# Kernel optimization log

Hardware: AMD Instinct MI355X
Metric: run time of the kernel (lower is better)

## Reference

```python
import jax, jax.numpy as jnp
import numpy as np

# Analytic closed form of the 4-qubit circuit. Wires (0,1) and (2,3) are
# independent 2-qubit blocks: RY(x_a)oRY(x_b) -> CNOT(a,b) -> RY(p_a)oRY(p_b).
# Heisenberg picture gives:
#   <Z_a> = cos(p_a)*cos(x_a) + sin(p_a)*sin(x_a)*sin(x_b)
#   <Z_b> = cos(p_b)*cos(x_a)*cos(x_b) + sin(p_b)*sin(x_b)

def setup_inputs() -> dict:
    key = jax.random.key(0)
    k1, k2, k3, k4 = jax.random.split(key, 4)
    B = 16384
    return {
        "x": jax.random.uniform(k1, (B, 1, 28, 28), dtype=jnp.float32),
        "vqc_params": jax.random.normal(k2, (4,), dtype=jnp.float32),
        "fc_w": jax.random.normal(k3, (10, 784), dtype=jnp.float32) * 0.05,
        "fc_b": jax.random.normal(k4, (10,), dtype=jnp.float32) * 0.05,
        "bias": jnp.zeros((10,), dtype=jnp.float32),
    }


def _pair_expvals(xa, xb, pa, pb):
    # xa, xb: [B, 196]; pa, pb: scalars
    za = jnp.cos(pa) * jnp.cos(xa) + jnp.sin(pa) * jnp.sin(xa) * jnp.sin(xb)
    zb = jnp.cos(pb) * jnp.cos(xa) * jnp.cos(xb) + jnp.sin(pb) * jnp.sin(xb)
    return za, zb


def reference(x, vqc_params, fc_w, fc_b, bias):
    B = x.shape[0]
    # Extract 2x2 patches in the same (r, c) row-major order as the torch loop.
    # [B,28,28] -> [B,14,2,14,2] -> [B,14,14,2,2] -> [B,196,4]
    p = x[:, 0].reshape(B, 14, 2, 14, 2).transpose(0, 1, 3, 2, 4).reshape(B, 196, 4)
    x0, x1, x2, x3 = p[..., 0], p[..., 1], p[..., 2], p[..., 3]
    p0, p1, p2, p3 = vqc_params[0], vqc_params[1], vqc_params[2], vqc_params[3]
    z0, z1 = _pair_expvals(x0, x1, p0, p1)
    z2, z3 = _pair_expvals(x2, x3, p2, p3)
    q = jnp.stack([z0, z1, z2, z3], axis=-1).reshape(B, 4 * 196)  # patch-major, wire-minor
    logits = q @ fc_w.T + fc_b - bias
    return jax.nn.log_softmax(logits, axis=-1)
```

## Files before the change

kernel.cpp:

```cpp
#include <hip/hip_runtime.h>
#include <hip/hip_bf16.h>


typedef __attribute__((ext_vector_type(8))) short short8;
typedef __attribute__((ext_vector_type(4))) float f32x4;

constexpr int WAVES = 4;
constexpr int BLOCK = WAVES * 64;
constexpr int IMGS  = 16;
constexpr int NITER = 7;

static __device__ __forceinline__ short f2bf(float f) {
    union { float f; unsigned u; } v; v.f = f;
    unsigned r = v.u + 0x7fffu + ((v.u >> 16) & 1u);
    return (short)(r >> 16);
}

__global__ __launch_bounds__(BLOCK, 4)
void quanv_mfma(const float* __restrict__ x,
                const float* __restrict__ vqc,
                const float* __restrict__ fc_w,
                const float* __restrict__ fc_b,
                const float* __restrict__ bias,
                float* __restrict__ out,
                int B)
{
    __shared__ float cpart[3][64 * 4];

    const int tid  = threadIdx.x;
    const int lane = tid & 63;
    const int wv   = tid >> 6;
    const int i16  = lane & 15;
    const int g    = lane >> 4;

    const int imgBase = blockIdx.x * IMGS;
    const int imgLane = imgBase + i16;
    const long xb = (long)(imgLane < B ? imgLane : B - 1) * 784;

    float S0, C0, S1, C1, S2, C2, S3, C3;
    __sincosf(vqc[0], &S0, &C0);
    __sincosf(vqc[1], &S1, &C1);
    __sincosf(vqc[2], &S2, &C2);
    __sincosf(vqc[3], &S3, &C3);

    const int ncl = (i16 < 10) ? i16 : 9;
    short8 bf[NITER];
    #pragma unroll
    for (int I = 0; I < NITER; ++I) {
        const int kb = wv + 4 * I;
        int k = kb * 32 + g * 8;
        if (k > 776) k = 776;
        const float4 lo = *reinterpret_cast<const float4*>(fc_w + ncl * 784 + k);
        const float4 hi = *reinterpret_cast<const float4*>(fc_w + ncl * 784 + k + 4);
        short8 t;
        t[0] = f2bf(lo.x); t[1] = f2bf(lo.y); t[2] = f2bf(lo.z); t[3] = f2bf(lo.w);
        t[4] = f2bf(hi.x); t[5] = f2bf(hi.y); t[6] = f2bf(hi.z); t[7] = f2bf(hi.w);
        bf[I] = t;
    }

    auto xoff = [&](int I) -> int {
        const int kb = wv + 4 * I;
        int j0 = kb * 8 + 2 * g;
        if (j0 > 194) j0 = 0;
        const int r = j0 / 14, c = j0 - 14 * r;
        return 56 * r + 2 * c;
    };

    f32x4 acc = {0.f, 0.f, 0.f, 0.f};

    float4 curT = *reinterpret_cast<const float4*>(x + xb + xoff(0));
    float4 curB = *reinterpret_cast<const float4*>(x + xb + xoff(0) + 28);

    #pragma unroll
    for (int I = 0; I < NITER; ++I) {
        float4 nxT, nxB;
        if (I < NITER - 1) {
            const int o = xoff(I + 1);
            nxT = *reinterpret_cast<const float4*>(x + xb + o);
            nxB = *reinterpret_cast<const float4*>(x + xb + o + 28);
        }

        const int   kb  = wv + 4 * I;
        const int   j0  = kb * 8 + 2 * g;
        const float msk = (j0 <= 194) ? 1.f : 0.f;

        float sA, cA, sB, cB, sC, cC, sD, cD;
        __sincosf(curT.x, &sA, &cA);  __sincosf(curT.y, &sB, &cB);
        __sincosf(curB.x, &sC, &cC);  __sincosf(curB.y, &sD, &cD);
        const float q0 = (C0 * cA + S0 * (sA * sB)) * msk;
        const float q1 = (C1 * (cA * cB) + S1 * sB) * msk;
        const float q2 = (C2 * cC + S2 * (sC * sD)) * msk;
        const float q3 = (C3 * (cC * cD) + S3 * sD) * msk;
        __sincosf(curT.z, &sA, &cA);  __sincosf(curT.w, &sB, &cB);
        __sincosf(curB.z, &sC, &cC);  __sincosf(curB.w, &sD, &cD);
        const float q4 = (C0 * cA + S0 * (sA * sB)) * msk;
        const float q5 = (C1 * (cA * cB) + S1 * sB) * msk;
        const float q6 = (C2 * cC + S2 * (sC * sD)) * msk;
        const float q7 = (C3 * (cC * cD) + S3 * sD) * msk;

        short8 a;
        a[0] = f2bf(q0); a[1] = f2bf(q1); a[2] = f2bf(q2); a[3] = f2bf(q3);
        a[4] = f2bf(q4); a[5] = f2bf(q5); a[6] = f2bf(q6); a[7] = f2bf(q7);

        acc = __builtin_amdgcn_mfma_f32_16x16x32_bf16(a, bf[I], acc, 0, 0, 0);

        curT = nxT; curB = nxB;
    }

    if (wv > 0)
        *reinterpret_cast<f32x4*>(&cpart[wv - 1][lane * 4]) = acc;
    __syncthreads();

    if (wv == 0) {
        #pragma unroll
        for (int p = 0; p < 3; ++p) {
            const f32x4 o = *reinterpret_cast<const f32x4*>(&cpart[p][lane * 4]);
            acc += o;
        }
        const float bk = (i16 < 10) ? (fc_b[i16] - bias[i16]) : 0.f;

        #pragma unroll
        for (int r = 0; r < 4; ++r) {
            const float lg = acc[r] + bk;
            float mx = (i16 < 10) ? lg : -3.0e38f;
            #pragma unroll
            for (int off = 1; off < 16; off <<= 1)
                mx = fmaxf(mx, __shfl_xor(mx, off, 64));
            float s = (i16 < 10) ? __expf(lg - mx) : 0.f;
            #pragma unroll
            for (int off = 1; off < 16; off <<= 1)
                s += __shfl_xor(s, off, 64);
            const int im = imgBase + g * 4 + r;
            if (i16 < 10 && im < B)
                out[(long)im * 10 + i16] = lg - mx - __logf(s);
        }
    }
}

extern "C" void kernel_launch(void* const* d_in, const int* in_sizes, int n_in,
                              void* d_out, int out_size, void* d_ws, size_t ws_size,
                              hipStream_t stream) {
    const float* x    = (const float*)d_in[0];
    const float* vqc  = (const float*)d_in[1];
    const float* fc_w = (const float*)d_in[2];
    const float* fc_b = (const float*)d_in[3];
    const float* bias = (const float*)d_in[4];
    float* outp = (float*)d_out;

    const int B = in_sizes[0] / 784;
    const int nblocks = (B + IMGS - 1) / IMGS;
    hipLaunchKernelGGL(quanv_mfma, dim3(nblocks), dim3(BLOCK), 0, stream,
                       x, vqc, fc_w, fc_b, bias, outp, B);
}
```

Measured before the change: 17.01 us.

## Read input pixels contiguously and permute fc_w columns to match

Each lane now reads 8 contiguous pixels along the image's row-major order instead of two 2x2 patch rows. The K ordering changes to follow raw pixel order, and the fc_w columns are gathered per pixel into the matching patch/wire index, with the VQC parameter pair chosen by row parity. Input loads are double-buffered two iterations ahead. This is meant to make the input stream contiguous, 32-byte aligned reads and to deepen prefetch. The cost is scattered float2 weight gathers and some per-iteration selects.

```diff
diff --git a/kernel.cpp b/kernel.cpp
--- a/kernel.cpp
+++ b/kernel.cpp
@@ -1,5 +1,4 @@
 #include <hip/hip_runtime.h>
-#include <hip/hip_bf16.h>
 
 
 typedef __attribute__((ext_vector_type(8))) short short8;
@@ -36,6 +35,15 @@
     const int imgBase = blockIdx.x * IMGS;
     const int imgLane = imgBase + i16;
     const long xb = (long)(imgLane < B ? imgLane : B - 1) * 784;
+    const int  k0 = wv * 32 + 8 * g;
+
+    const float* __restrict__ xp = x + xb + k0;
+
+    float4 bufA[2], bufB[2];
+    bufA[0] = *reinterpret_cast<const float4*>(xp);
+    bufB[0] = *reinterpret_cast<const float4*>(xp + 4);
+    bufA[1] = *reinterpret_cast<const float4*>(xp + 128);
+    bufB[1] = *reinterpret_cast<const float4*>(xp + 132);
 
     float S0, C0, S1, C1, S2, C2, S3, C3;
     __sincosf(vqc[0], &S0, &C0);
@@ -44,67 +52,74 @@
     __sincosf(vqc[3], &S3, &C3);
 
     const int ncl = (i16 < 10) ? i16 : 9;
+    const float* __restrict__ wrow = fc_w + ncl * 784;
     short8 bf[NITER];
     #pragma unroll
     for (int I = 0; I < NITER; ++I) {
-        const int kb = wv + 4 * I;
-        int k = kb * 32 + g * 8;
-        if (k > 776) k = 776;
-        const float4 lo = *reinterpret_cast<const float4*>(fc_w + ncl * 784 + k);
-        const float4 hi = *reinterpret_cast<const float4*>(fc_w + ncl * 784 + k + 4);
         short8 t;
-        t[0] = f2bf(lo.x); t[1] = f2bf(lo.y); t[2] = f2bf(lo.z); t[3] = f2bf(lo.w);
-        t[4] = f2bf(hi.x); t[5] = f2bf(hi.y); t[6] = f2bf(hi.z); t[7] = f2bf(hi.w);
+        #pragma unroll
+        for (int u = 0; u < 4; ++u) {
+            int pix = k0 + 128 * I + 2 * u;
+            pix = pix < 782 ? pix : 782;
+            const int y  = pix / 28;
+            const int c  = pix - 28 * y;
+            const int qp = ((y >> 1) * 14 + (c >> 1)) * 4 + (y & 1) * 2;
+            const float2 w2 = *reinterpret_cast<const float2*>(wrow + qp);
+            t[2 * u]     = f2bf(w2.x);
+            t[2 * u + 1] = f2bf(w2.y);
+        }
         bf[I] = t;
     }
 
-    auto xoff = [&](int I) -> int {
-        const int kb = wv + 4 * I;
-        int j0 = kb * 8 + 2 * g;
-        if (j0 > 194) j0 = 0;
-        const int r = j0 / 14, c = j0 - 14 * r;
-        return 56 * r + 2 * c;
-    };
-
     f32x4 acc = {0.f, 0.f, 0.f, 0.f};
-
-    float4 curT = *reinterpret_cast<const float4*>(x + xb + xoff(0));
-    float4 curB = *reinterpret_cast<const float4*>(x + xb + xoff(0) + 28);
+    int rr = k0 % 28;
+    int pi = (k0 / 28) & 1;
 
     #pragma unroll
     for (int I = 0; I < NITER; ++I) {
-        float4 nxT, nxB;
-        if (I < NITER - 1) {
-            const int o = xoff(I + 1);
-            nxT = *reinterpret_cast<const float4*>(x + xb + o);
-            nxB = *reinterpret_cast<const float4*>(x + xb + o + 28);
+        const float4 a4 = bufA[I & 1];
+        const float4 b4 = bufB[I & 1];
+
+        if (I + 2 <= NITER - 2) {
+            bufA[I & 1] = *reinterpret_cast<const float4*>(xp + 128 * (I + 2));
+            bufB[I & 1] = *reinterpret_cast<const float4*>(xp + 128 * (I + 2) + 4);
+        } else if (I + 2 == NITER - 1) {
+            const int kl = (k0 + 128 * (NITER - 1) <= 776) ? 128 * (NITER - 1)
+                                                           : 776 - k0;
+            bufA[I & 1] = *reinterpret_cast<const float4*>(xp + kl);
+            bufB[I & 1] = *reinterpret_cast<const float4*>(xp + kl + 4);
         }
 
-        const int   kb  = wv + 4 * I;
-        const int   j0  = kb * 8 + 2 * g;
-        const float msk = (j0 <= 194) ? 1.f : 0.f;
-
-        float sA, cA, sB, cB, sC, cC, sD, cD;
-        __sincosf(curT.x, &sA, &cA);  __sincosf(curT.y, &sB, &cB);
-        __sincosf(curB.x, &sC, &cC);  __sincosf(curB.y, &sD, &cD);
-        const float q0 = (C0 * cA + S0 * (sA * sB)) * msk;
-        const float q1 = (C1 * (cA * cB) + S1 * sB) * msk;
-        const float q2 = (C2 * cC + S2 * (sC * sD)) * msk;
-        const float q3 = (C3 * (cC * cD) + S3 * sD) * msk;
-        __sincosf(curT.z, &sA, &cA);  __sincosf(curT.w, &sB, &cB);
-        __sincosf(curB.z, &sC, &cC);  __sincosf(curB.w, &sD, &cD);
-        const float q4 = (C0 * cA + S0 * (sA * sB)) * msk;
-        const float q5 = (C1 * (cA * cB) + S1 * sB) * msk;
-        const float q6 = (C2 * cC + S2 * (sC * sD)) * msk;
-        const float q7 = (C3 * (cC * cD) + S3 * sD) * msk;
+        float q[8];
+        #pragma unroll
+        for (int u = 0; u < 4; ++u) {
+            const float xa = (u == 0) ? a4.x : (u == 1) ? a4.z
+                           : (u == 2) ? b4.x : b4.z;
+            const float xv = (u == 0) ? a4.y : (u == 1) ? a4.w
+                           : (u == 2) ? b4.y : b4.w;
+            const int   pu = pi ^ ((rr + 2 * u) >= 28);
+            const float CA = pu ? C2 : C0, SA = pu ? S2 : S0;
+            const float CB = pu ? C3 : C1, SB = pu ? S3 : S1;
+            float sa, ca, sb, cb;
+            __sincosf(xa, &sa, &ca);
+            __sincosf(xv, &sb, &cb);
+            float za = CA * ca + SA * (sa * sb);
+            float zb = CB * (ca * cb) + SB * sb;
+            if (I == NITER - 1) {
+                const float m = (k0 + 128 * I + 2 * u) < 784 ? 1.f : 0.f;
+                za *= m; zb *= m;
+            }
+            q[2 * u]     = za;
+            q[2 * u + 1] = zb;
+        }
+        rr += 16;
+        if (rr >= 28) { rr -= 28; pi ^= 1; }
 
         short8 a;
-        a[0] = f2bf(q0); a[1] = f2bf(q1); a[2] = f2bf(q2); a[3] = f2bf(q3);
-        a[4] = f2bf(q4); a[5] = f2bf(q5); a[6] = f2bf(q6); a[7] = f2bf(q7);
+        #pragma unroll
+        for (int e = 0; e < 8; ++e) a[e] = f2bf(q[e]);
 
         acc = __builtin_amdgcn_mfma_f32_16x16x32_bf16(a, bf[I], acc, 0, 0, 0);
-
-        curT = nxT; curB = nxB;
     }
 
     if (wv > 0)
@@ -113,10 +128,8 @@
 
     if (wv == 0) {
         #pragma unroll
-        for (int p = 0; p < 3; ++p) {
-            const f32x4 o = *reinterpret_cast<const f32x4*>(&cpart[p][lane * 4]);
-            acc += o;
-        }
+        for (int p = 0; p < 3; ++p)
+            acc += *reinterpret_cast<const f32x4*>(&cpart[p][lane * 4]);
         const float bk = (i16 < 10) ? (fc_b[i16] - bias[i16]) : 0.f;
 
         #pragma unroll
```

Result: slower. 20.65 us (+21.4%).
